# Kernel optimization log

Hardware: AMD Instinct MI355X
Metric: run time of the kernel (lower is better)

## Reference

```python
import jax, jax.numpy as jnp
import numpy as np

H = 1152  # hidden_size
NH = 16   # num_attention_heads
HD = H // NH  # head_dim = 72
FF = 4304  # intermediate_size
EPS = 1e-6
S = 4096
B = 1
NDOCS = 32


def _linear_params(key, d_in, d_out):
    kw, kb = jax.random.split(key)
    lim = 1.0 / np.sqrt(d_in)
    w = jax.random.uniform(kw, (d_out, d_in), jnp.float32, -lim, lim)
    b = jax.random.uniform(kb, (d_out,), jnp.float32, -lim, lim)
    return w, b


def setup_inputs() -> dict:
    key = jax.random.key(0)
    ks = jax.random.split(key, 8)
    hidden_states = jax.random.normal(ks[0], (B, S, H), jnp.float32)
    document_ids = jnp.sort(jax.random.randint(ks[1], (S,), 0, NDOCS))
    q_w, q_b = _linear_params(ks[2], H, H)
    k_w, k_b = _linear_params(ks[3], H, H)
    v_w, v_b = _linear_params(ks[4], H, H)
    o_w, o_b = _linear_params(ks[5], H, H)
    fc1_w, fc1_b = _linear_params(ks[6], H, FF)
    fc2_w, fc2_b = _linear_params(ks[7], FF, H)
    return {
        'hidden_states': hidden_states,
        'document_ids': document_ids,
        'q_w': q_w, 'q_b': q_b, 'k_w': k_w, 'k_b': k_b,
        'v_w': v_w, 'v_b': v_b, 'o_w': o_w, 'o_b': o_b,
        'ln1_g': jnp.ones((H,), jnp.float32), 'ln1_b': jnp.zeros((H,), jnp.float32),
        'ln2_g': jnp.ones((H,), jnp.float32), 'ln2_b': jnp.zeros((H,), jnp.float32),
        'fc1_w': fc1_w, 'fc1_b': fc1_b, 'fc2_w': fc2_w, 'fc2_b': fc2_b,
    }


def _layer_norm(x, g, b):
    mu = jnp.mean(x, axis=-1, keepdims=True)
    var = jnp.mean(jnp.square(x - mu), axis=-1, keepdims=True)
    return (x - mu) * jax.lax.rsqrt(var + EPS) * g + b


def _forward(hidden_states, q_w, q_b, k_w, k_b, v_w, v_b, o_w, o_b,
             ln1_g, ln1_b, ln2_g, ln2_b, fc1_w, fc1_b, fc2_w, fc2_b,
             document_ids):
    b, s, _ = hidden_states.shape
    scale = HD ** -0.5

    residual = hidden_states
    x = _layer_norm(hidden_states, ln1_g, ln1_b)

    # projections (torch Linear: y = x @ W.T + b)
    q = (x @ q_w.T + q_b).reshape(b, s, NH, HD).transpose(0, 2, 1, 3)
    k = (x @ k_w.T + k_b).reshape(b, s, NH, HD).transpose(0, 2, 1, 3)
    v = (x @ v_w.T + v_b).reshape(b, s, NH, HD).transpose(0, 2, 1, 3)

    # document-masked attention: attend only within same document id
    scores = jnp.einsum('bhqd,bhkd->bhqk', q, k) * scale
    mask = document_ids[:, None] == document_ids[None, :]  # [s, s]
    scores = jnp.where(mask[None, None], scores, -jnp.inf)
    attn = jax.nn.softmax(scores, axis=-1)
    out = jnp.einsum('bhqk,bhkd->bhqd', attn, v)  # [b,h,s,d]
    out = out.transpose(0, 2, 1, 3).reshape(b, s, H)
    out = out @ o_w.T + o_b

    hidden = residual + out
    residual = hidden
    x = _layer_norm(hidden, ln2_g, ln2_b)
    x = jax.nn.gelu(x @ fc1_w.T + fc1_b, approximate=True)
    x = x @ fc2_w.T + fc2_b
    return residual + x


def reference(hidden_states, document_ids, q_w, q_b, k_w, k_b, v_w, v_b,
              o_w, o_b, ln1_g, ln1_b, ln2_g, ln2_b, fc1_w, fc1_b, fc2_w, fc2_b):
    return _forward(hidden_states, q_w, q_b, k_w, k_b, v_w, v_b, o_w, o_b,
                    ln1_g, ln1_b, ln2_g, ln2_b, fc1_w, fc1_b, fc2_w, fc2_b,
                    document_ids)
```

## Files before the change

kernel.cpp:

```cpp
#include <hip/hip_runtime.h>

typedef unsigned short u16;
typedef unsigned int u32;
typedef __attribute__((ext_vector_type(8))) __bf16 bf16x8;
typedef __attribute__((ext_vector_type(8))) u16 u16x8;
typedef __attribute__((ext_vector_type(4))) float f32x4;
typedef __attribute__((ext_vector_type(2))) u32 u32x2;

#define SEQ 4096
#define HID 1152
#define NHEAD 16
#define HDIM 72
#define FF 4304
#define FFP 4352
#define H3 3456

__device__ __forceinline__ u16 f2bf(float f) {
  u32 u = __builtin_bit_cast(u32, f);
  u32 r = u + 0x7fffu + ((u >> 16) & 1u);
  return (u16)(r >> 16);
}
__device__ __forceinline__ float bf2f(u16 h) {
  return __builtin_bit_cast(float, (u32)h << 16);
}

typedef const __attribute__((address_space(1))) void* gas_t;
typedef __attribute__((address_space(3))) void* las_t;
__device__ __forceinline__ void load_lds16(const void* g, void* l) {
  __builtin_amdgcn_global_load_lds((gas_t)(unsigned long long)g,
                                   (las_t)(u32)(unsigned long long)l, 16, 0, 0);
}

__device__ __forceinline__ float gelu_tanh(float x) {
  float t = tanhf(0.7978845608f * (x + 0.044715f * x * x * x));
  return 0.5f * x * (1.f + t);
}

__global__ __launch_bounds__(256) void cvt4_k(const float* __restrict__ in,
                                              u16* __restrict__ out, int n4) {
  int i = blockIdx.x * 256 + threadIdx.x;
  if (i >= n4) return;
  f32x4 f = ((const f32x4*)in)[i];
  u32x2 o;
  o[0] = (u32)f2bf(f[0]) | ((u32)f2bf(f[1]) << 16);
  o[1] = (u32)f2bf(f[2]) | ((u32)f2bf(f[3]) << 16);
  ((u32x2*)out)[i] = o;
}

__global__ __launch_bounds__(256) void cvt4_pad_k(const float* __restrict__ in,
                                                  u16* __restrict__ out,
                                                  int rows, int sc, int dc) {
  int i = blockIdx.x * 256 + threadIdx.x;
  long long n4 = (long long)rows * dc / 4;
  if (i >= n4) return;
  long long idx = (long long)i * 4;
  int r = (int)(idx / dc);
  int c = (int)(idx % dc);
  u32x2 o;
  if (c < sc) {
    f32x4 f = *(const f32x4*)(in + (size_t)r * sc + c);
    o[0] = (u32)f2bf(f[0]) | ((u32)f2bf(f[1]) << 16);
    o[1] = (u32)f2bf(f[2]) | ((u32)f2bf(f[3]) << 16);
  } else {
    o[0] = 0; o[1] = 0;
  }
  ((u32x2*)out)[i] = o;
}

__global__ __launch_bounds__(256) void pack_bias_k(const float* __restrict__ qb,
                                                   const float* __restrict__ kb,
                                                   const float* __restrict__ vb,
                                                   const float* __restrict__ f1b,
                                                   float* __restrict__ bqkv,
                                                   float* __restrict__ bf1,
                                                   float* __restrict__ zbuf) {
  int i = blockIdx.x * 256 + threadIdx.x;
  if (i < H3) bqkv[i] = (i < HID) ? qb[i] : (i < 2 * HID ? kb[i - HID] : vb[i - 2 * HID]);
  if (i < FFP) bf1[i] = (i < FF) ? f1b[i] : 0.f;
  if (i < 16) zbuf[i] = 0.f;
}

__global__ __launch_bounds__(256) void docrange_k(const int* __restrict__ ids,
                                                  int* __restrict__ se) {
  int i = blockIdx.x * 256 + threadIdx.x;
  if (i >= SEQ) return;
  int id = ids[i];
  int lo = 0, hi = SEQ;
  while (lo < hi) { int mid = (lo + hi) >> 1; if (ids[mid] < id) lo = mid + 1; else hi = mid; }
  int s = lo;
  lo = 0; hi = SEQ;
  while (lo < hi) { int mid = (lo + hi) >> 1; if (ids[mid] <= id) lo = mid + 1; else hi = mid; }
  se[2 * i] = s;
  se[2 * i + 1] = lo;
}

__global__ __launch_bounds__(256) void ln_k(const float* __restrict__ x,
                                            const float* __restrict__ g,
                                            const float* __restrict__ b,
                                            u16* __restrict__ y) {
  __shared__ float sred[8];
  int row = blockIdx.x, tid = threadIdx.x;
  const f32x4* xr = (const f32x4*)(x + (size_t)row * HID);
  f32x4 v0 = {}, v1 = {};
  float s = 0.f, s2 = 0.f;
  int c0 = tid, c1 = tid + 256;
  v0 = xr[c0];
  if (c1 < 288) v1 = xr[c1];
#pragma unroll
  for (int j = 0; j < 4; ++j) { s += v0[j] + v1[j]; s2 += v0[j] * v0[j] + v1[j] * v1[j]; }
#pragma unroll
  for (int sh = 32; sh; sh >>= 1) { s += __shfl_xor(s, sh); s2 += __shfl_xor(s2, sh); }
  if ((tid & 63) == 0) { sred[tid >> 6] = s; sred[4 + (tid >> 6)] = s2; }
  __syncthreads();
  s = sred[0] + sred[1] + sred[2] + sred[3];
  s2 = sred[4] + sred[5] + sred[6] + sred[7];
  float mu = s * (1.f / HID);
  float rs = rsqrtf(s2 * (1.f / HID) - mu * mu + 1e-6f);
  u16* yr = y + (size_t)row * HID;
  const f32x4* g4 = (const f32x4*)g;
  const f32x4* b4 = (const f32x4*)b;
  {
    f32x4 gv = g4[c0], bv = b4[c0];
    u32x2 o;
    o[0] = (u32)f2bf((v0[0] - mu) * rs * gv[0] + bv[0]) |
           ((u32)f2bf((v0[1] - mu) * rs * gv[1] + bv[1]) << 16);
    o[1] = (u32)f2bf((v0[2] - mu) * rs * gv[2] + bv[2]) |
           ((u32)f2bf((v0[3] - mu) * rs * gv[3] + bv[3]) << 16);
    *(u32x2*)(yr + c0 * 4) = o;
  }
  if (c1 < 288) {
    f32x4 gv = g4[c1], bv = b4[c1];
    u32x2 o;
    o[0] = (u32)f2bf((v1[0] - mu) * rs * gv[0] + bv[0]) |
           ((u32)f2bf((v1[1] - mu) * rs * gv[1] + bv[1]) << 16);
    o[1] = (u32)f2bf((v1[2] - mu) * rs * gv[2] + bv[2]) |
           ((u32)f2bf((v1[3] - mu) * rs * gv[3] + bv[3]) << 16);
    *(u32x2*)(yr + c1 * 4) = o;
  }
}

template <int EP>
__global__ __launch_bounds__(256, 2) void gemm_bt(const u16* __restrict__ A,
                                                  const u16* __restrict__ B,
                                                  void* __restrict__ outp,
                                                  const float* __restrict__ bias,
                                                  const float* __restrict__ resid,
                                                  int M, int N, int K) {
  __shared__ u16 As[128 * 32];
  __shared__ u16 Bs[128 * 32];
  int tid = threadIdx.x;
  int l = tid & 63, w = tid >> 6;
  int m0 = blockIdx.y * 128, n0 = blockIdx.x * 128;
  int wr = w >> 1, wc = w & 1;
  f32x4 acc[4][4] = {};
  int offr = tid >> 2;
  int offc = (tid & 3) * 16;
  const char* Ab0 = (const char*)A + ((size_t)(m0 + offr) * K) * 2 + offc;
  const char* Ab1 = (const char*)A + ((size_t)(m0 + 64 + offr) * K) * 2 + offc;
  const char* Bb0 = (const char*)B + ((size_t)(n0 + offr) * K) * 2 + offc;
  const char* Bb1 = (const char*)B + ((size_t)(n0 + 64 + offr) * K) * 2 + offc;
  char* AsW = (char*)As + w * 1024;
  char* BsW = (char*)Bs + w * 1024;
  const char* Ar = (const char*)As + (wr * 64 + (l & 15)) * 64 + (l >> 4) * 16;
  const char* Br = (const char*)Bs + (wc * 64 + (l & 15)) * 64 + (l >> 4) * 16;
  for (int kt = 0; kt < K; kt += 32) {
    size_t kb = (size_t)kt * 2;
    load_lds16(Ab0 + kb, AsW);
    load_lds16(Ab1 + kb, AsW + 4096);
    load_lds16(Bb0 + kb, BsW);
    load_lds16(Bb1 + kb, BsW + 4096);
    __syncthreads();
    bf16x8 af[4], bfr[4];
#pragma unroll
    for (int m = 0; m < 4; ++m) af[m] = *(const bf16x8*)(Ar + m * 16 * 64);
#pragma unroll
    for (int n = 0; n < 4; ++n) bfr[n] = *(const bf16x8*)(Br + n * 16 * 64);
#pragma unroll
    for (int m = 0; m < 4; ++m)
#pragma unroll
      for (int n = 0; n < 4; ++n)
        acc[m][n] = __builtin_amdgcn_mfma_f32_16x16x32_bf16(af[m], bfr[n], acc[m][n], 0, 0, 0);
    __syncthreads();
  }
#pragma unroll
  for (int m = 0; m < 4; ++m) {
    int row = m0 + wr * 64 + m * 16 + (l >> 4) * 4;
#pragma unroll
    for (int n = 0; n < 4; ++n) {
      int col = n0 + wc * 64 + n * 16 + (l & 15);
      float bv = bias[col];
      if (EP == 4) {
        int region = (col >= 2304) ? 2 : (col >= 1152 ? 1 : 0);
        int cw = col - region * 1152;
        int hh = cw / 72;
        int dd = cw - hh * 72;
        u16* dst = (u16*)outp + (((size_t)region * NHEAD + hh) * SEQ) * HDIM + dd;
#pragma unroll
        for (int j = 0; j < 4; ++j)
          dst[(size_t)(row + j) * HDIM] = f2bf(acc[m][n][j] + bv);
      } else {
#pragma unroll
        for (int j = 0; j < 4; ++j) {
          size_t idx = (size_t)(row + j) * N + col;
          float v = acc[m][n][j] + bv;
          if (EP == 1) ((u16*)outp)[idx] = f2bf(gelu_tanh(v));
          else ((float*)outp)[idx] = v + resid[idx];
        }
      }
    }
  }
}

__device__ __forceinline__ u32 swz(u32 a) { return a ^ (((a >> 8) & 7u) << 4); }

__global__ __launch_bounds__(256, 2) void attn_mfma_k(const u16* __restrict__ qkvh,
                                                      const int* __restrict__ se,
                                                      const float* __restrict__ zb,
                                                      u16* __restrict__ outb) {
  __shared__ u16 Ks[128 * 104];
  __shared__ u16 Vt[80 * 128];
  __shared__ u16 Ps[4][16 * 128];
  __shared__ int Sq[64], Eq[64];
  int tid = threadIdx.x, l = tid & 63, w = tid >> 6;
  int h = blockIdx.y, q0 = blockIdx.x * 64;
  const float scale = 0.1178511302f;
  const u16* Qh = qkvh + (size_t)h * SEQ * HDIM;
  const u16* Kh = qkvh + ((size_t)NHEAD + h) * SEQ * HDIM;
  const u16* Vh = qkvh + ((size_t)2 * NHEAD + h) * SEQ * HDIM;

  for (int i = tid; i < 512; i += 256) ((u32*)(Vt + 72 * 128))[i] = 0;

#pragma unroll
  for (int it = 0; it < 4; ++it) {
    int cw0 = it * 256 + w * 64;
    if (cw0 < 832) {
      int chunk = cw0 + l;
      int row = chunk / 13, c16 = chunk - row * 13;
      const void* src = (c16 < 9)
                            ? (const void*)(Qh + ((size_t)(q0 + row)) * HDIM + c16 * 8)
                            : (const void*)zb;
      load_lds16(src, (char*)Ks + (size_t)cw0 * 16);
    }
  }
  if (tid < 64) { Sq[tid] = se[2 * (q0 + tid)]; Eq[tid] = se[2 * (q0 + tid) + 1]; }
  __syncthreads();

  int sqj[4], eqj[4];
#pragma unroll
  for (int j = 0; j < 4; ++j) {
    int ql = w * 16 + (l >> 4) * 4 + j;
    sqj[j] = Sq[ql]; eqj[j] = Eq[ql];
  }
  const char* Aq = (const char*)Ks + (w * 16 + (l & 15)) * 208 + (l >> 4) * 16;
  bf16x8 aq[3];
#pragma unroll
  for (int dsl = 0; dsl < 3; ++dsl) aq[dsl] = *(const bf16x8*)(Aq + dsl * 64);
  __syncthreads();

  int kmin = se[2 * q0];
  int kmax = se[2 * (q0 + 63) + 1];
  f32x4 o[5] = {};
  float m_run[4], l_run[4];
#pragma unroll
  for (int j = 0; j < 4; ++j) { m_run[j] = -1e30f; l_run[j] = 0.f; }

  for (int kc = kmin; kc < kmax; kc += 128) {
#pragma unroll
    for (int it = 0; it < 7; ++it) {
      int cw0 = it * 256 + w * 64;
      if (cw0 < 1664) {
        int chunk = cw0 + l;
        int row = chunk / 13, c16 = chunk - row * 13;
        int krow = kc + row;
        const void* src = (c16 < 9 && krow < SEQ)
                              ? (const void*)(Kh + (size_t)krow * HDIM + c16 * 8)
                              : (const void*)zb;
        load_lds16(src, (char*)Ks + (size_t)cw0 * 16);
      }
    }
#pragma unroll
    for (int it = 0; it < 3; ++it) {
      int idx = it * 256 + tid;
      if (idx < 576) {
        int k2 = idx / 9, d8 = idx - k2 * 9;
        int kr0 = kc + 2 * k2, kr1 = kr0 + 1;
        kr0 = kr0 < SEQ ? kr0 : SEQ - 1;
        kr1 = kr1 < SEQ ? kr1 : SEQ - 1;
        u16x8 r0 = *(const u16x8*)(Vh + (size_t)kr0 * HDIM + d8 * 8);
        u16x8 r1 = *(const u16x8*)(Vh + (size_t)kr1 * HDIM + d8 * 8);
#pragma unroll
        for (int j = 0; j < 8; ++j) {
          u32 pr = (u32)r0[j] | ((u32)r1[j] << 16);
          *(u32*)((char*)Vt + swz((u32)(d8 * 8 + j) * 256 + (u32)k2 * 4)) = pr;
        }
      }
    }
    __syncthreads();

    f32x4 sf[8];
#pragma unroll
    for (int kt = 0; kt < 8; ++kt) {
      const char* Bk = (const char*)Ks + (kt * 16 + (l & 15)) * 208 + (l >> 4) * 16;
      f32x4 acc = {};
      acc = __builtin_amdgcn_mfma_f32_16x16x32_bf16(aq[0], *(const bf16x8*)Bk, acc, 0, 0, 0);
      acc = __builtin_amdgcn_mfma_f32_16x16x32_bf16(aq[1], *(const bf16x8*)(Bk + 64), acc, 0, 0, 0);
      acc = __builtin_amdgcn_mfma_f32_16x16x32_bf16(aq[2], *(const bf16x8*)(Bk + 128), acc, 0, 0, 0);
      sf[kt] = acc;
    }
    float mx[4] = {-1e30f, -1e30f, -1e30f, -1e30f};
#pragma unroll
    for (int kt = 0; kt < 8; ++kt) {
      int key = kc + kt * 16 + (l & 15);
#pragma unroll
      for (int j = 0; j < 4; ++j) {
        float s = sf[kt][j] * scale;
        bool valid = (key >= sqj[j]) && (key < eqj[j]);
        s = valid ? s : -1e30f;
        sf[kt][j] = s;
        mx[j] = fmaxf(mx[j], s);
      }
    }
#pragma unroll
    for (int j = 0; j < 4; ++j) {
      float m = mx[j];
      m = fmaxf(m, __shfl_xor(m, 1));
      m = fmaxf(m, __shfl_xor(m, 2));
      m = fmaxf(m, __shfl_xor(m, 4));
      m = fmaxf(m, __shfl_xor(m, 8));
      mx[j] = m;
    }
    float fz[4], ps[4];
#pragma unroll
    for (int j = 0; j < 4; ++j) {
      float mn = fmaxf(m_run[j], mx[j]);
      fz[j] = __expf(m_run[j] - mn);
      m_run[j] = mn;
      ps[j] = 0.f;
    }
#pragma unroll
    for (int kt = 0; kt < 8; ++kt)
#pragma unroll
      for (int j = 0; j < 4; ++j) {
        float s = sf[kt][j];
        float p = (s > -1e29f) ? __expf(s - m_run[j]) : 0.f;
        sf[kt][j] = p;
        ps[j] += p;
      }
#pragma unroll
    for (int j = 0; j < 4; ++j) {
      float p = ps[j];
      p += __shfl_xor(p, 1);
      p += __shfl_xor(p, 2);
      p += __shfl_xor(p, 4);
      p += __shfl_xor(p, 8);
      l_run[j] = l_run[j] * fz[j] + p;
#pragma unroll
      for (int dt = 0; dt < 5; ++dt) o[dt][j] *= fz[j];
    }
    char* PB = (char*)Ps[w];
#pragma unroll
    for (int kt = 0; kt < 8; ++kt)
#pragma unroll
      for (int j = 0; j < 4; ++j) {
        u32 a = (u32)((l >> 4) * 4 + j) * 256 + (u32)(kt * 16 + (l & 15)) * 2;
        *(u16*)(PB + swz(a)) = f2bf(sf[kt][j]);
      }
#pragma unroll
    for (int ks = 0; ks < 4; ++ks) {
      u32 aa = (u32)(l & 15) * 256 + (u32)((l >> 4) * 8 + ks * 32) * 2;
      bf16x8 ap = *(const bf16x8*)(PB + swz(aa));
#pragma unroll
      for (int dt = 0; dt < 5; ++dt) {
        u32 ba = (u32)(dt * 16 + (l & 15)) * 256 + (u32)((l >> 4) * 8 + ks * 32) * 2;
        bf16x8 bv = *(const bf16x8*)((const char*)Vt + swz(ba));
        o[dt] = __builtin_amdgcn_mfma_f32_16x16x32_bf16(ap, bv, o[dt], 0, 0, 0);
      }
    }
    __syncthreads();
  }

  float inv[4];
#pragma unroll
  for (int j = 0; j < 4; ++j) inv[j] = 1.f / l_run[j];
#pragma unroll
  for (int dt = 0; dt < 5; ++dt) {
    int d = dt * 16 + (l & 15);
    if (d < HDIM) {
#pragma unroll
      for (int j = 0; j < 4; ++j) {
        int q = q0 + w * 16 + (l >> 4) * 4 + j;
        outb[(size_t)q * HID + h * HDIM + d] = f2bf(o[dt][j] * inv[j]);
      }
    }
  }
}

constexpr size_t SZ_WQKV = (size_t)H3 * HID * 2;
constexpr size_t SZ_WO   = (size_t)HID * HID * 2;
constexpr size_t SZ_WF1  = (size_t)FFP * HID * 2;
constexpr size_t SZ_WF2  = (size_t)HID * FFP * 2;
constexpr size_t OFF_WQKV = 0;
constexpr size_t OFF_WO   = OFF_WQKV + SZ_WQKV;
constexpr size_t OFF_WF1  = OFF_WO + SZ_WO;
constexpr size_t OFF_WF2  = OFF_WF1 + SZ_WF1;
constexpr size_t OFF_BQKV = OFF_WF2 + SZ_WF2;
constexpr size_t OFF_BF1  = OFF_BQKV + (size_t)H3 * 4;
constexpr size_t OFF_SE   = OFF_BF1 + (size_t)FFP * 4;
constexpr size_t OFF_ZB   = OFF_SE + (size_t)SEQ * 2 * 4;
constexpr size_t OFF_XLN  = OFF_ZB + 64;
constexpr size_t OFF_QKV  = OFF_XLN + (size_t)SEQ * HID * 2;
constexpr size_t OFF_ACT  = OFF_QKV;
constexpr size_t OFF_AOUT = OFF_QKV + (size_t)SEQ * H3 * 2;
constexpr size_t OFF_HD   = OFF_AOUT + (size_t)SEQ * HID * 2;
constexpr size_t WS_NEED  = OFF_HD + (size_t)SEQ * HID * 4;
static_assert(OFF_ACT + (size_t)SEQ * FFP * 2 <= OFF_HD, "ACT must not clobber HD");

extern "C" void kernel_launch(void* const* d_in, const int* in_sizes, int n_in,
                              void* d_out, int out_size, void* d_ws, size_t ws_size,
                              hipStream_t stream) {
  const float* hs   = (const float*)d_in[0];
  const int*   ids  = (const int*)d_in[1];
  const float* q_w  = (const float*)d_in[2];
  const float* q_b  = (const float*)d_in[3];
  const float* k_w  = (const float*)d_in[4];
  const float* k_b  = (const float*)d_in[5];
  const float* v_w  = (const float*)d_in[6];
  const float* v_b  = (const float*)d_in[7];
  const float* o_w  = (const float*)d_in[8];
  const float* o_b  = (const float*)d_in[9];
  const float* ln1g = (const float*)d_in[10];
  const float* ln1b = (const float*)d_in[11];
  const float* ln2g = (const float*)d_in[12];
  const float* ln2b = (const float*)d_in[13];
  const float* f1w  = (const float*)d_in[14];
  const float* f1b  = (const float*)d_in[15];
  const float* f2w  = (const float*)d_in[16];
  const float* f2b  = (const float*)d_in[17];

  if (ws_size < WS_NEED) return;

  char* ws = (char*)d_ws;
  u16*   Wqkv = (u16*)(ws + OFF_WQKV);
  u16*   Wo   = (u16*)(ws + OFF_WO);
  u16*   Wf1  = (u16*)(ws + OFF_WF1);
  u16*   Wf2  = (u16*)(ws + OFF_WF2);
  float* Bqkv = (float*)(ws + OFF_BQKV);
  float* Bf1  = (float*)(ws + OFF_BF1);
  int*   SE   = (int*)(ws + OFF_SE);
  float* ZB   = (float*)(ws + OFF_ZB);
  u16*   XLN  = (u16*)(ws + OFF_XLN);
  u16*   QKVh = (u16*)(ws + OFF_QKV);
  u16*   ACT  = (u16*)(ws + OFF_ACT);
  u16*   AOUT = (u16*)(ws + OFF_AOUT);
  float* HD   = (float*)(ws + OFF_HD);

  docrange_k<<<dim3(SEQ / 256), dim3(256), 0, stream>>>(ids, SE);

  int nW = HID * HID;
  cvt4_k<<<dim3((nW / 4 + 255) / 256), dim3(256), 0, stream>>>(q_w, Wqkv, nW / 4);
  cvt4_k<<<dim3((nW / 4 + 255) / 256), dim3(256), 0, stream>>>(k_w, Wqkv + nW, nW / 4);
  cvt4_k<<<dim3((nW / 4 + 255) / 256), dim3(256), 0, stream>>>(v_w, Wqkv + 2 * nW, nW / 4);
  cvt4_k<<<dim3((nW / 4 + 255) / 256), dim3(256), 0, stream>>>(o_w, Wo, nW / 4);
  {
    int n4 = FFP * HID / 4;
    cvt4_pad_k<<<dim3((n4 + 255) / 256), dim3(256), 0, stream>>>(f1w, Wf1, 1, FF * HID, FFP * HID);
  }
  {
    int n4 = HID * FFP / 4;
    cvt4_pad_k<<<dim3((n4 + 255) / 256), dim3(256), 0, stream>>>(f2w, Wf2, HID, FF, FFP);
  }
  pack_bias_k<<<dim3((FFP + 255) / 256), dim3(256), 0, stream>>>(q_b, k_b, v_b, f1b, Bqkv, Bf1, ZB);

  ln_k<<<dim3(SEQ), dim3(256), 0, stream>>>(hs, ln1g, ln1b, XLN);
  gemm_bt<4><<<dim3(H3 / 128, SEQ / 128), dim3(256), 0, stream>>>(XLN, Wqkv, QKVh, Bqkv, nullptr,
                                                                  SEQ, H3, HID);
  attn_mfma_k<<<dim3(SEQ / 64, NHEAD), dim3(256), 0, stream>>>(QKVh, SE, ZB, AOUT);
  gemm_bt<2><<<dim3(HID / 128, SEQ / 128), dim3(256), 0, stream>>>(AOUT, Wo, HD, o_b, hs,
                                                                   SEQ, HID, HID);
  ln_k<<<dim3(SEQ), dim3(256), 0, stream>>>(HD, ln2g, ln2b, XLN);
  gemm_bt<1><<<dim3(FFP / 128, SEQ / 128), dim3(256), 0, stream>>>(XLN, Wf1, ACT, Bf1, nullptr,
                                                                   SEQ, FFP, HID);
  gemm_bt<3><<<dim3(HID / 128, SEQ / 128), dim3(256), 0, stream>>>(ACT, Wf2, (float*)d_out, f2b, HD,
                                                                   SEQ, HID, FFP);
}
```

Measured before the change: 351.5 us.

## Split-K the FC2 GEMM with bf16 partials and add XCD-aware block remapping

The FC2 GEMM (K=4352, only 288 output tiles) is split three ways along K. Each split writes bf16 partial sums into a dead workspace region, and a separate reduce kernel adds the partials, bias and residual. This raises the block count to fill more CUs. All gemm_bt launches also remap block IDs so consecutive tiles land on the same XCD, aiming for better L2 reuse. The cost is an extra kernel, extra partial-sum traffic, and precision loss from rounding partials to bf16. The workspace layout is reshuffled to fit the partials.

```diff
diff --git a/kernel.cpp b/kernel.cpp
--- a/kernel.cpp
+++ b/kernel.cpp
@@ -23,6 +23,8 @@
 __device__ __forceinline__ float bf2f(u16 h) {
   return __builtin_bit_cast(float, (u32)h << 16);
 }
+__device__ __forceinline__ float bflo(u32 u) { return __builtin_bit_cast(float, u << 16); }
+__device__ __forceinline__ float bfhi(u32 u) { return __builtin_bit_cast(float, u & 0xffff0000u); }
 
 typedef const __attribute__((address_space(1))) void* gas_t;
 typedef __attribute__((address_space(3))) void* las_t;
@@ -150,7 +152,12 @@
   __shared__ u16 Bs[128 * 32];
   int tid = threadIdx.x;
   int l = tid & 63, w = tid >> 6;
-  int m0 = blockIdx.y * 128, n0 = blockIdx.x * 128;
+  int nxy = gridDim.x * gridDim.y;
+  int bidf = blockIdx.y * gridDim.x + blockIdx.x;
+  int cpx = nxy >> 3;
+  bidf = (bidf & 7) * cpx + (bidf >> 3);
+  int m0 = (bidf / gridDim.x) * 128;
+  int n0 = (bidf % gridDim.x) * 128;
   int wr = w >> 1, wc = w & 1;
   f32x4 acc[4][4] = {};
   int offr = tid >> 2;
@@ -163,7 +170,14 @@
   char* BsW = (char*)Bs + w * 1024;
   const char* Ar = (const char*)As + (wr * 64 + (l & 15)) * 64 + (l >> 4) * 16;
   const char* Br = (const char*)Bs + (wc * 64 + (l & 15)) * 64 + (l >> 4) * 16;
-  for (int kt = 0; kt < K; kt += 32) {
+  int k0 = 0, kend = K;
+  if (EP == 5) {
+    int nz = gridDim.z;
+    int ksp = ((K / 32 + nz - 1) / nz) * 32;
+    k0 = blockIdx.z * ksp;
+    kend = min(K, k0 + ksp);
+  }
+  for (int kt = k0; kt < kend; kt += 32) {
     size_t kb = (size_t)kt * 2;
     load_lds16(Ab0 + kb, AsW);
     load_lds16(Ab1 + kb, AsW + 4096);
@@ -188,7 +202,7 @@
 #pragma unroll
     for (int n = 0; n < 4; ++n) {
       int col = n0 + wc * 64 + n * 16 + (l & 15);
-      float bv = bias[col];
+      float bv = (EP == 5) ? 0.f : bias[col];
       if (EP == 4) {
         int region = (col >= 2304) ? 2 : (col >= 1152 ? 1 : 0);
         int cw = col - region * 1152;
@@ -198,6 +212,11 @@
 #pragma unroll
         for (int j = 0; j < 4; ++j)
           dst[(size_t)(row + j) * HDIM] = f2bf(acc[m][n][j] + bv);
+      } else if (EP == 5) {
+        u16* P = (u16*)outp + (size_t)blockIdx.z * M * N;
+#pragma unroll
+        for (int j = 0; j < 4; ++j)
+          P[(size_t)(row + j) * N + col] = f2bf(acc[m][n][j]);
       } else {
 #pragma unroll
         for (int j = 0; j < 4; ++j) {
@@ -209,6 +228,29 @@
       }
     }
   }
+}
+
+template <int NS>
+__global__ __launch_bounds__(256) void splitk_reduce_k(const u16* __restrict__ P,
+                                                       const float* __restrict__ bias,
+                                                       const float* __restrict__ resid,
+                                                       float* __restrict__ out, int n4) {
+  int i = blockIdx.x * 256 + threadIdx.x;
+  if (i >= n4) return;
+  size_t base = (size_t)i * 4;
+  int col = (int)(base % HID);
+  f32x4 a = {};
+#pragma unroll
+  for (int s = 0; s < NS; ++s) {
+    u32x2 pv = *(const u32x2*)(P + (size_t)s * SEQ * HID + base);
+    a[0] += bflo(pv[0]);
+    a[1] += bfhi(pv[0]);
+    a[2] += bflo(pv[1]);
+    a[3] += bfhi(pv[1]);
+  }
+  f32x4 bv = *(const f32x4*)(bias + col);
+  f32x4 rv = ((const f32x4*)resid)[i];
+  ((f32x4*)out)[i] = a + bv + rv;
 }
 
 __device__ __forceinline__ u32 swz(u32 a) { return a ^ (((a >> 8) & 7u) << 4); }
@@ -402,8 +444,7 @@
 constexpr size_t OFF_WQKV = 0;
 constexpr size_t OFF_WO   = OFF_WQKV + SZ_WQKV;
 constexpr size_t OFF_WF1  = OFF_WO + SZ_WO;
-constexpr size_t OFF_WF2  = OFF_WF1 + SZ_WF1;
-constexpr size_t OFF_BQKV = OFF_WF2 + SZ_WF2;
+constexpr size_t OFF_BQKV = OFF_WF1 + SZ_WF1;
 constexpr size_t OFF_BF1  = OFF_BQKV + (size_t)H3 * 4;
 constexpr size_t OFF_SE   = OFF_BF1 + (size_t)FFP * 4;
 constexpr size_t OFF_ZB   = OFF_SE + (size_t)SEQ * 2 * 4;
@@ -412,8 +453,11 @@
 constexpr size_t OFF_ACT  = OFF_QKV;
 constexpr size_t OFF_AOUT = OFF_QKV + (size_t)SEQ * H3 * 2;
 constexpr size_t OFF_HD   = OFF_AOUT + (size_t)SEQ * HID * 2;
-constexpr size_t WS_NEED  = OFF_HD + (size_t)SEQ * HID * 4;
+constexpr size_t OFF_WF2  = OFF_HD + (size_t)SEQ * HID * 4;
+constexpr size_t WS_NEED  = OFF_WF2 + SZ_WF2;
+constexpr size_t OFF_P    = 0;
 static_assert(OFF_ACT + (size_t)SEQ * FFP * 2 <= OFF_HD, "ACT must not clobber HD");
+static_assert(3 * (size_t)SEQ * HID * 2 <= OFF_QKV, "P must stay in dead prefix");
 
 extern "C" void kernel_launch(void* const* d_in, const int* in_sizes, int n_in,
                               void* d_out, int out_size, void* d_ws, size_t ws_size,
@@ -453,6 +497,7 @@
   u16*   ACT  = (u16*)(ws + OFF_ACT);
   u16*   AOUT = (u16*)(ws + OFF_AOUT);
   float* HD   = (float*)(ws + OFF_HD);
+  u16*   Pp   = (u16*)(ws + OFF_P);
 
   docrange_k<<<dim3(SEQ / 256), dim3(256), 0, stream>>>(ids, SE);
 
@@ -480,6 +525,9 @@
   ln_k<<<dim3(SEQ), dim3(256), 0, stream>>>(HD, ln2g, ln2b, XLN);
   gemm_bt<1><<<dim3(FFP / 128, SEQ / 128), dim3(256), 0, stream>>>(XLN, Wf1, ACT, Bf1, nullptr,
                                                                    SEQ, FFP, HID);
-  gemm_bt<3><<<dim3(HID / 128, SEQ / 128), dim3(256), 0, stream>>>(ACT, Wf2, (float*)d_out, f2b, HD,
-                                                                   SEQ, HID, FFP);
-}
+  gemm_bt<5><<<dim3(HID / 128, SEQ / 128, 3), dim3(256), 0, stream>>>(ACT, Wf2, Pp, nullptr,
+                                                                      nullptr, SEQ, HID, FFP);
+  splitk_reduce_k<3><<<dim3(SEQ * HID / 4 / 256), dim3(256), 0, stream>>>(Pp, f2b, HD,
+                                                                          (float*)d_out,
+                                                                          SEQ * HID / 4);
+}
```

New measurement: 312.5 us. 1.12x faster.
